# Performance work log

Hardware: AMD Instinct MI355X
Metric: run time of the kernel (lower is better)

Reference implementation:

```python
import jax, jax.numpy as jnp
import numpy as np

VOCAB, HIDDEN, BATCH, SEQ = 32000, 512, 64, 512


def setup_inputs() -> dict:
    key = jax.random.key(0)
    k0, k1, k2, k3, k4, k5 = jax.random.split(key, 6)
    s = 1.0 / np.sqrt(HIDDEN)  # PyTorch LSTMCell init scale
    return {
        "inputs": jax.random.randint(k0, (BATCH, SEQ), 0, VOCAB, dtype=jnp.int64),
        "embedding": jax.random.normal(k1, (VOCAB, HIDDEN), dtype=jnp.float32),
        "W_ih": jax.random.normal(k2, (4 * HIDDEN, HIDDEN), dtype=jnp.float32) * s,
        "W_hh": jax.random.normal(k3, (4 * HIDDEN, HIDDEN), dtype=jnp.float32) * s,
        "b_ih": jax.random.normal(k4, (4 * HIDDEN,), dtype=jnp.float32) * s,
        "b_hh": jax.random.normal(k5, (4 * HIDDEN,), dtype=jnp.float32) * s,
    }


def reference(inputs, embedding, W_ih, W_hh, b_ih, b_hh):
    # Embedding lookup: (B, S, H)
    x = embedding[inputs]
    B, S, H = x.shape
    bias = b_ih + b_hh

    def step(carry, xt):
        h, c = carry
        # gates: (B, 4H); PyTorch LSTMCell gate order i, f, g, o
        gates = xt @ W_ih.T + h @ W_hh.T + bias
        i, f, g, o = jnp.split(gates, 4, axis=-1)
        i = jax.nn.sigmoid(i)
        f = jax.nn.sigmoid(f)
        g = jnp.tanh(g)
        o = jax.nn.sigmoid(o)
        c_new = f * c + i * g
        h_new = o * jnp.tanh(c_new)
        return (h_new, c_new), h_new

    h0 = jnp.zeros((B, H), dtype=x.dtype)
    c0 = jnp.zeros((B, H), dtype=x.dtype)
    (h, c), hs = jax.lax.scan(step, (h0, c0), jnp.swapaxes(x, 0, 1))
    annotations = jnp.swapaxes(hs, 0, 1)  # (B, S, H)
    return annotations, h, c
```

## Files before the change

kernel.cpp:

```cpp
#include <hip/hip_runtime.h>
#include <math.h>

#define B 64
#define S 512
#define H 512
#define G4 2048

typedef __attribute__((ext_vector_type(8))) short bf16x8;
typedef __attribute__((ext_vector_type(4))) float f32x4;

__device__ __forceinline__ float sigmoidf_(float x) {
    return 1.0f / (1.0f + __expf(-x));
}
__device__ __forceinline__ float tanhf_(float x) {
    return 2.0f / (1.0f + __expf(-2.0f * x)) - 1.0f;
}

__device__ __forceinline__ ushort f2bf(float f) {
    union { float f; unsigned int u; } v; v.f = f;
    unsigned int r = v.u + 0x7FFFu + ((v.u >> 16) & 1u);
    return (ushort)(r >> 16);
}
__device__ __forceinline__ float bf2f(ushort s) {
    union { unsigned int u; float f; } v; v.u = ((unsigned int)s) << 16;
    return v.f;
}
__device__ __forceinline__ void split_bf(float x, ushort& hi, ushort& lo) {
    const ushort h = f2bf(x);
    hi = h;
    lo = f2bf(x - bf2f(h));
}

__global__ __launch_bounds__(256)
void w_split(const float* __restrict__ W,
             ushort* __restrict__ Whi,
             ushort* __restrict__ Wlo)
{
    const int i = blockIdx.x * 256 + threadIdx.x;
    const float4 v = reinterpret_cast<const float4*>(W)[i];
    ushort4 hi, lo;
    split_bf(v.x, hi.x, lo.x);
    split_bf(v.y, hi.y, lo.y);
    split_bf(v.z, hi.z, lo.z);
    split_bf(v.w, hi.w, lo.w);
    reinterpret_cast<ushort4*>(Whi)[i] = hi;
    reinterpret_cast<ushort4*>(Wlo)[i] = lo;
}

__global__ __launch_bounds__(256)
void xg_mfma(const int* __restrict__ tokens,
             const float* __restrict__ emb,
             const ushort* __restrict__ Whi,
             const ushort* __restrict__ Wlo,
             const float* __restrict__ b_ih,
             const float* __restrict__ b_hh,
             ushort* __restrict__ xg)
{
    const int mtile = blockIdx.x;
    const int ntile = blockIdx.y;
    const int tid   = threadIdx.x;

    __shared__ ushort Ahi[128][32];
    __shared__ ushort Alo[128][32];
    __shared__ ushort Bhi[128][32];
    __shared__ ushort Blo[128][32];

    const int ar  = tid >> 3;
    const int seg = tid & 7;
    const float* asrc[4];
    #pragma unroll
    for (int i = 0; i < 4; ++i) {
        const int m   = mtile * 128 + ar + i * 32;
        const int tok = tokens[(m & 63) * S + (m >> 6)];
        asrc[i] = emb + (size_t)tok * H + seg * 4;
    }

    const int br = tid >> 2;
    const int bc = (tid & 3) * 8;
    const ushort* bsrc_hi[2];
    const ushort* bsrc_lo[2];
    #pragma unroll
    for (int j = 0; j < 2; ++j) {
        const int n = ntile * 128 + br + j * 64;
        bsrc_hi[j] = Whi + (size_t)n * H + bc;
        bsrc_lo[j] = Wlo + (size_t)n * H + bc;
    }

    const int lane = tid & 63;
    const int wv   = tid >> 6;
    const int wr   = (wv >> 1) * 64;
    const int wc   = (wv & 1) * 64;
    const int fr   = lane & 15;
    const int ks   = lane >> 4;

    f32x4 acc[4][4];
    #pragma unroll
    for (int a = 0; a < 4; ++a)
        #pragma unroll
        for (int c = 0; c < 4; ++c)
            acc[a][c] = (f32x4){0.f, 0.f, 0.f, 0.f};

    for (int kc = 0; kc < 16; ++kc) {
        const int d0 = kc * 32;

        #pragma unroll
        for (int i = 0; i < 4; ++i) {
            const float4 v = *reinterpret_cast<const float4*>(asrc[i] + d0);
            ushort4 hi, lo;
            split_bf(v.x, hi.x, lo.x);
            split_bf(v.y, hi.y, lo.y);
            split_bf(v.z, hi.z, lo.z);
            split_bf(v.w, hi.w, lo.w);
            const int r = ar + i * 32;
            *reinterpret_cast<ushort4*>(&Ahi[r][seg * 4]) = hi;
            *reinterpret_cast<ushort4*>(&Alo[r][seg * 4]) = lo;
        }
        #pragma unroll
        for (int j = 0; j < 2; ++j) {
            const int r = br + j * 64;
            *reinterpret_cast<uint4*>(&Bhi[r][bc]) =
                *reinterpret_cast<const uint4*>(bsrc_hi[j] + d0);
            *reinterpret_cast<uint4*>(&Blo[r][bc]) =
                *reinterpret_cast<const uint4*>(bsrc_lo[j] + d0);
        }
        __syncthreads();

        bf16x8 ah[4], al[4];
        #pragma unroll
        for (int fm = 0; fm < 4; ++fm) {
            ah[fm] = *reinterpret_cast<const bf16x8*>(&Ahi[wr + fm * 16 + fr][ks * 8]);
            al[fm] = *reinterpret_cast<const bf16x8*>(&Alo[wr + fm * 16 + fr][ks * 8]);
        }
        #pragma unroll
        for (int fn = 0; fn < 4; ++fn) {
            const bf16x8 bh = *reinterpret_cast<const bf16x8*>(&Bhi[wc + fn * 16 + fr][ks * 8]);
            const bf16x8 bl = *reinterpret_cast<const bf16x8*>(&Blo[wc + fn * 16 + fr][ks * 8]);
            #pragma unroll
            for (int fm = 0; fm < 4; ++fm) {
                acc[fm][fn] = __builtin_amdgcn_mfma_f32_16x16x32_bf16(ah[fm], bh, acc[fm][fn], 0, 0, 0);
                acc[fm][fn] = __builtin_amdgcn_mfma_f32_16x16x32_bf16(al[fm], bh, acc[fm][fn], 0, 0, 0);
                acc[fm][fn] = __builtin_amdgcn_mfma_f32_16x16x32_bf16(ah[fm], bl, acc[fm][fn], 0, 0, 0);
            }
        }
        __syncthreads();
    }

    #pragma unroll
    for (int fn = 0; fn < 4; ++fn) {
        const int col  = ntile * 128 + wc + fn * 16 + fr;
        const float bias = b_ih[col] + b_hh[col];
        const int gate = col >> 9;
        const int k    = col & 511;
        const int w    = k >> 4;
        const int kl   = k & 15;
        #pragma unroll
        for (int fm = 0; fm < 4; ++fm) {
            const int row = mtile * 128 + wr + fm * 16 + ks * 4;
            const int t   = row >> 6;
            const int b   = row & 63;
            const int g   = b >> 3;
            const int b8  = b & 7;
            ushort4 us;
            us.x = f2bf(acc[fm][fn][0] + bias);
            us.y = f2bf(acc[fm][fn][1] + bias);
            us.z = f2bf(acc[fm][fn][2] + bias);
            us.w = f2bf(acc[fm][fn][3] + bias);
            const size_t idx = ((((size_t)t * 8 + g) * 32 + w) * 512) +
                               gate * 128 + kl * 8 + b8;
            *reinterpret_cast<ushort4*>(&xg[idx]) = us;
        }
    }
}

__global__ __launch_bounds__(256)
void xg_gemm(const int* __restrict__ tokens,
             const float* __restrict__ emb,
             const float* __restrict__ W_ih,
             const float* __restrict__ b_ih,
             const float* __restrict__ b_hh,
             ushort* __restrict__ xg)
{
    const int t      = blockIdx.x;
    const int g_base = blockIdx.y * 128;
    const int tid    = threadIdx.x;

    const int b_ld = tid >> 2;
    const int seg  = tid & 3;
    const int r_w  = tid >> 1;
    const int half = tid & 1;
    const int b0 = (tid & 15) * 4;
    const int g0 = (tid >> 4) * 8;

    const int token = tokens[b_ld * S + t];
    const float4* embrow = reinterpret_cast<const float4*>(emb) + (size_t)token * (H / 4);

    __shared__ float hs[64][64];
    __shared__ float ws[128][68];

    float acc[4][8];
    #pragma unroll
    for (int i = 0; i < 4; ++i)
        #pragma unroll
        for (int j = 0; j < 8; ++j) acc[i][j] = 0.0f;

    for (int kc = 0; kc < 8; ++kc) {
        const int d0 = kc * 64;
        #pragma unroll
        for (int i = 0; i < 4; ++i) {
            const int dl = seg * 16 + i * 4;
            const float4 f = embrow[(d0 >> 2) + seg * 4 + i];
            hs[dl + 0][b_ld] = f.x;
            hs[dl + 1][b_ld] = f.y;
            hs[dl + 2][b_ld] = f.z;
            hs[dl + 3][b_ld] = f.w;
        }
        const float4* wrow = reinterpret_cast<const float4*>(W_ih) +
                             (size_t)(g_base + r_w) * (H / 4) + (d0 >> 2) + half * 8;
        #pragma unroll
        for (int i = 0; i < 8; ++i) {
            *reinterpret_cast<float4*>(&ws[r_w][half * 32 + i * 4]) = wrow[i];
        }
        __syncthreads();

        #pragma unroll
        for (int d4 = 0; d4 < 16; ++d4) {
            const float4 hv0 = *reinterpret_cast<const float4*>(&hs[d4 * 4 + 0][b0]);
            const float4 hv1 = *reinterpret_cast<const float4*>(&hs[d4 * 4 + 1][b0]);
            const float4 hv2 = *reinterpret_cast<const float4*>(&hs[d4 * 4 + 2][b0]);
            const float4 hv3 = *reinterpret_cast<const float4*>(&hs[d4 * 4 + 3][b0]);
            #pragma unroll
            for (int gg = 0; gg < 8; ++gg) {
                const float4 w = *reinterpret_cast<const float4*>(&ws[g0 + gg][d4 * 4]);
                acc[0][gg] += hv0.x * w.x + hv1.x * w.y + hv2.x * w.z + hv3.x * w.w;
                acc[1][gg] += hv0.y * w.x + hv1.y * w.y + hv2.y * w.z + hv3.y * w.w;
                acc[2][gg] += hv0.z * w.x + hv1.z * w.y + hv2.z * w.z + hv3.z * w.w;
                acc[3][gg] += hv0.w * w.x + hv1.w * w.y + hv2.w * w.z + hv3.w * w.w;
            }
        }
        __syncthreads();
    }

    const int grp = b0 >> 3;
    const int b8l = b0 & 7;
    #pragma unroll
    for (int gg = 0; gg < 8; ++gg) {
        const int gcol = g_base + g0 + gg;
        const int gate = gcol >> 9;
        const int k    = gcol & 511;
        const int w    = k >> 4;
        const int kl   = k & 15;
        const float bias = b_ih[gcol] + b_hh[gcol];
        ushort4 us;
        us.x = f2bf(acc[0][gg] + bias);
        us.y = f2bf(acc[1][gg] + bias);
        us.z = f2bf(acc[2][gg] + bias);
        us.w = f2bf(acc[3][gg] + bias);
        const size_t idx = ((((size_t)t * 8 + grp) * 32 + w) * 512) +
                           gate * 128 + kl * 8 + b8l;
        *reinterpret_cast<ushort4*>(&xg[idx]) = us;
    }
}

#define GSTR 4096
#define PSTR 32768

__global__ __launch_bounds__(256)
__attribute__((amdgpu_waves_per_eu(1, 1)))
void lstm_persist_mfma(const ushort* __restrict__ Whh_hi,
                       const ushort* __restrict__ Whh_lo,
                       const ushort* __restrict__ xg,
                       float* __restrict__ hq,
                       unsigned int* __restrict__ bar,
                       float* __restrict__ out)
{
    const int tid  = threadIdx.x;
    const int g    = blockIdx.x & 7;
    const int w    = blockIdx.x >> 3;
    const int k0   = w * 16;
    const int lane = tid & 63;
    const int wv   = tid >> 6;

    unsigned int* bcnt = bar + g * 64;

    const int  bcol   = lane & 15;
    const int  klane  = 4 * wv + (lane >> 4);
    const bool active = bcol < 8;
    const int  b8     = lane & 7;

    const ushort* xg_wg = xg + (((size_t)g * 32 + w) * 512);

    const int ar    = lane & 15;
    const int agate = ar & 3;
    const int ak    = k0 + 4 * wv + (ar >> 2);
    const size_t arow = ((size_t)agate * 512 + ak) * 512 + (size_t)(lane >> 4) * 8;
    bf16x8 afh[16], afl[16];
    #pragma unroll
    for (int ks = 0; ks < 16; ++ks) {
        afh[ks] = *reinterpret_cast<const bf16x8*>(Whh_hi + arow + ks * 32);
        afl[ks] = *reinterpret_cast<const bf16x8*>(Whh_lo + arow + ks * 32);
    }

    __shared__ ushort hs_hi[8 * 512];
    __shared__ ushort hs_lo[8 * 512];

    float c_reg = 0.0f;

    float xv_cur[4] = {0.f, 0.f, 0.f, 0.f};
    if (active) {
        #pragma unroll
        for (int gate = 0; gate < 4; ++gate)
            xv_cur[gate] = bf2f(xg_wg[gate * 128 + klane * 8 + b8]);
    }

    char* hs_hi_c = reinterpret_cast<char*>(hs_hi);
    char* hs_lo_c = reinterpret_cast<char*>(hs_lo);

    for (int t = 0; t < S; ++t) {
        const unsigned long long* hsrc8 = reinterpret_cast<const unsigned long long*>(
            hq + (t & 1) * PSTR + g * GSTR);
        unsigned long long hv[8];
        #pragma unroll
        for (int i = 0; i < 8; ++i)
            hv[i] = __hip_atomic_load(&hsrc8[i * 256 + tid],
                                      __ATOMIC_RELAXED, __HIP_MEMORY_SCOPE_AGENT);
        #pragma unroll
        for (int i = 0; i < 8; ++i) {
            const int e  = 2 * (i * 256 + tid);
            const int bb = e >> 9;
            const int dd = e & 511;
            union { unsigned long long u; float f[2]; } uv; uv.u = hv[i];
            ushort h0, l0, h1, l1;
            split_bf(uv.f[0], h0, l0);
            split_bf(uv.f[1], h1, l1);
            const int byteoff = ((bb << 10) + (dd << 1)) ^ (bb << 4);
            *reinterpret_cast<unsigned int*>(hs_hi_c + byteoff) =
                ((unsigned int)h1 << 16) | (unsigned int)h0;
            *reinterpret_cast<unsigned int*>(hs_lo_c + byteoff) =
                ((unsigned int)l1 << 16) | (unsigned int)l0;
        }
        __syncthreads();

        float xv_nxt[4] = {0.f, 0.f, 0.f, 0.f};
        if (active && t + 1 < S) {
            const ushort* p = xg_wg + (size_t)(t + 1) * (8 * 32 * 512);
            #pragma unroll
            for (int gate = 0; gate < 4; ++gate)
                xv_nxt[gate] = bf2f(p[gate * 128 + klane * 8 + b8]);
        }

        f32x4 a0 = (f32x4){0.f,0.f,0.f,0.f}, a1 = a0, a2 = a0, a3 = a0, a4 = a0, a5 = a0;
        #pragma unroll
        for (int ks = 0; ks < 16; ++ks) {
            const int kbyte = ((b8 << 10) + ((ks * 32 + (lane >> 4) * 8) << 1)) ^ (b8 << 4);
            const bf16x8 bh = *reinterpret_cast<const bf16x8*>(hs_hi_c + kbyte);
            const bf16x8 bl = *reinterpret_cast<const bf16x8*>(hs_lo_c + kbyte);
            if (ks & 1) {
                a1 = __builtin_amdgcn_mfma_f32_16x16x32_bf16(afh[ks], bh, a1, 0, 0, 0);
                a3 = __builtin_amdgcn_mfma_f32_16x16x32_bf16(afl[ks], bh, a3, 0, 0, 0);
                a5 = __builtin_amdgcn_mfma_f32_16x16x32_bf16(afh[ks], bl, a5, 0, 0, 0);
            } else {
                a0 = __builtin_amdgcn_mfma_f32_16x16x32_bf16(afh[ks], bh, a0, 0, 0, 0);
                a2 = __builtin_amdgcn_mfma_f32_16x16x32_bf16(afl[ks], bh, a2, 0, 0, 0);
                a4 = __builtin_amdgcn_mfma_f32_16x16x32_bf16(afh[ks], bl, a4, 0, 0, 0);
            }
        }
        const f32x4 acc = (a0 + a1) + ((a2 + a3) + (a4 + a5));

        float hn = 0.0f, cn = 0.0f;
        if (active) {
            const float ig = sigmoidf_(acc[0] + xv_cur[0]);
            const float fg = sigmoidf_(acc[1] + xv_cur[1]);
            const float gg = tanhf_(acc[2] + xv_cur[2]);
            const float og = sigmoidf_(acc[3] + xv_cur[3]);
            cn = fg * c_reg + ig * gg;
            c_reg = cn;
            hn = og * tanhf_(cn);
            __hip_atomic_store(&hq[((t & 1) ^ 1) * PSTR + g * GSTR + b8 * 512 + k0 + klane],
                               hn, __ATOMIC_RELAXED, __HIP_MEMORY_SCOPE_AGENT);
        }

        __syncthreads();
        if (tid == 0)
            __hip_atomic_fetch_add(bcnt, 1u, __ATOMIC_RELAXED,
                                   __HIP_MEMORY_SCOPE_AGENT);

        if (active) {
            out[((size_t)(g * 8 + b8) * S + t) * H + k0 + klane] = hn;
            if (t == S - 1) {
                const size_t OFF = (size_t)B * S * H;
                out[OFF + (size_t)(g * 8 + b8) * H + k0 + klane] = hn;
                out[OFF + (size_t)B * H + (size_t)(g * 8 + b8) * H + k0 + klane] = cn;
            }
        }

        const unsigned int target = 32u * (unsigned int)(t + 1);
        while (__hip_atomic_load(bcnt, __ATOMIC_RELAXED,
                                 __HIP_MEMORY_SCOPE_AGENT) < target)
            __builtin_amdgcn_s_sleep(2);

        xv_cur[0] = xv_nxt[0]; xv_cur[1] = xv_nxt[1];
        xv_cur[2] = xv_nxt[2]; xv_cur[3] = xv_nxt[3];
    }
}

__global__ __launch_bounds__(256)
__attribute__((amdgpu_waves_per_eu(1, 1)))
void lstm_persist(const float* __restrict__ W_hh,
                  const ushort* __restrict__ xg,
                  float* __restrict__ hq,
                  unsigned int* __restrict__ bar,
                  float* __restrict__ out)
{
    const int tid = threadIdx.x;
    const int g   = blockIdx.x & 7;
    const int w   = blockIdx.x >> 3;
    const int k0  = w * 16;

    const int rp = tid & 31;
    const int d8 = tid >> 5;
    const int d0 = d8 * 64;

    const int b8 = tid >> 4;
    const int kl = tid & 15;

    unsigned int* bcnt = bar + g * 64;

    const ushort* xg_wg = xg + (((size_t)g * 32 + w) * 512);

    float4 wreg[2][16];
    #pragma unroll
    for (int r = 0; r < 2; ++r) {
        const int rl = 2 * rp + r;
        const int grow = (rl >> 4) * H + k0 + (rl & 15);
        const float4* wp = reinterpret_cast<const float4*>(W_hh + (size_t)grow * H + d0);
        #pragma unroll
        for (int i = 0; i < 16; ++i) wreg[r][i] = wp[i];
    }

    __shared__ float hs[8 * 512];
    __shared__ float part[8 * 8 * 64];

    float c_reg = 0.0f;

    float xv_cur[4] = {0.f, 0.f, 0.f, 0.f};
    if (tid < 128) {
        #pragma unroll
        for (int gate = 0; gate < 4; ++gate)
            xv_cur[gate] = bf2f(xg_wg[gate * 128 + kl * 8 + b8]);
    }

    for (int t = 0; t < S; ++t) {
        const unsigned long long* hsrc8 = reinterpret_cast<const unsigned long long*>(
            hq + (t & 1) * PSTR + g * GSTR);
        #pragma unroll
        for (int i = 0; i < 8; ++i) {
            const unsigned long long v = __hip_atomic_load(&hsrc8[i * 256 + tid],
                                                           __ATOMIC_RELAXED,
                                                           __HIP_MEMORY_SCOPE_AGENT);
            reinterpret_cast<unsigned long long*>(hs)[i * 256 + tid] = v;
        }
        __syncthreads();

        float xv_nxt[4] = {0.f, 0.f, 0.f, 0.f};
        if (tid < 128 && t + 1 < S) {
            const ushort* p = xg_wg + (size_t)(t + 1) * (8 * 32 * 512);
            #pragma unroll
            for (int gate = 0; gate < 4; ++gate)
                xv_nxt[gate] = bf2f(p[gate * 128 + kl * 8 + b8]);
        }

        float acc[2][8];
        #pragma unroll
        for (int r = 0; r < 2; ++r)
            #pragma unroll
            for (int b = 0; b < 8; ++b) acc[r][b] = 0.0f;

        #pragma unroll
        for (int b = 0; b < 8; ++b) {
            const float4* h4 = reinterpret_cast<const float4*>(hs + b * 512 + d0);
            #pragma unroll
            for (int i = 0; i < 16; ++i) {
                const float4 hv = h4[i];
                acc[0][b] += wreg[0][i].x * hv.x + wreg[0][i].y * hv.y +
                             wreg[0][i].z * hv.z + wreg[0][i].w * hv.w;
                acc[1][b] += wreg[1][i].x * hv.x + wreg[1][i].y * hv.y +
                             wreg[1][i].z * hv.z + wreg[1][i].w * hv.w;
            }
        }

        #pragma unroll
        for (int r = 0; r < 2; ++r)
            #pragma unroll
            for (int b = 0; b < 8; ++b)
                part[d8 * 512 + b * 64 + 2 * rp + r] = acc[r][b];
        __syncthreads();

        if (tid < 128) {
            float v[4];
            #pragma unroll
            for (int gate = 0; gate < 4; ++gate) {
                const int rl = gate * 16 + kl;
                float s = 0.0f;
                #pragma unroll
                for (int q = 0; q < 8; ++q) s += part[q * 512 + b8 * 64 + rl];
                v[gate] = s + xv_cur[gate];
            }
            const float ig = sigmoidf_(v[0]);
            const float fg = sigmoidf_(v[1]);
            const float gg = tanhf_(v[2]);
            const float og = sigmoidf_(v[3]);

            const float cn = fg * c_reg + ig * gg;
            c_reg = cn;
            const float hn = og * tanhf_(cn);

            __hip_atomic_store(&hq[((t & 1) ^ 1) * PSTR + g * GSTR + b8 * 512 + k0 + kl],
                               hn, __ATOMIC_RELAXED, __HIP_MEMORY_SCOPE_AGENT);
            out[((size_t)(g * 8 + b8) * S + t) * H + k0 + kl] = hn;
            if (t == S - 1) {
                const size_t OFF = (size_t)B * S * H;
                out[OFF + (size_t)(g * 8 + b8) * H + k0 + kl] = hn;
                out[OFF + (size_t)B * H + (size_t)(g * 8 + b8) * H + k0 + kl] = cn;
            }
        }

        __syncthreads();
        if (tid == 0) {
            __hip_atomic_fetch_add(bcnt, 1u, __ATOMIC_RELAXED,
                                   __HIP_MEMORY_SCOPE_AGENT);
            const unsigned int target = 32u * (unsigned int)(t + 1);
            while (__hip_atomic_load(bcnt, __ATOMIC_RELAXED,
                                     __HIP_MEMORY_SCOPE_AGENT) < target)
                __builtin_amdgcn_s_sleep(2);
        }
        __syncthreads();

        xv_cur[0] = xv_nxt[0]; xv_cur[1] = xv_nxt[1];
        xv_cur[2] = xv_nxt[2]; xv_cur[3] = xv_nxt[3];
    }
}

__global__ __launch_bounds__(128)
void lstm_step_fb(const int* __restrict__ tokens,
                  const float* __restrict__ emb,
                  const float* __restrict__ W_ih,
                  const float* __restrict__ W_hh,
                  const float* __restrict__ b_ih,
                  const float* __restrict__ b_hh,
                  const float* __restrict__ h_prev,
                  float* __restrict__ h_next,
                  float* __restrict__ c_st,
                  float* __restrict__ out,
                  int t)
{
    const int tid = threadIdx.x;
    const int b   = tid & 63;
    const int k   = blockIdx.x * 2 + (tid >> 6);
    const int token = tokens[b * S + t];
    const float* xrow = emb + (size_t)token * H;
    const float* hrow = h_prev + b * H;
    float acc[4];
    #pragma unroll
    for (int g = 0; g < 4; ++g) acc[g] = b_ih[g * H + k] + b_hh[g * H + k];
    for (int d = 0; d < H; ++d) {
        const float xv = xrow[d], hv = hrow[d];
        #pragma unroll
        for (int g = 0; g < 4; ++g)
            acc[g] += xv * W_ih[(size_t)(g * H + k) * H + d] + hv * W_hh[(size_t)(g * H + k) * H + d];
    }
    const float ig = sigmoidf_(acc[0]);
    const float fg = sigmoidf_(acc[1]);
    const float gg = tanhf(acc[2]);
    const float og = sigmoidf_(acc[3]);
    const int ck = b * H + k;
    const float cn = fg * c_st[ck] + ig * gg;
    c_st[ck] = cn;
    const float hn = og * tanhf(cn);
    h_next[ck] = hn;
    out[(size_t)b * S * H + (size_t)t * H + k] = hn;
    if (t == S - 1) {
        out[(size_t)B * S * H + ck] = hn;
        out[(size_t)B * S * H + B * H + ck] = cn;
    }
}

extern "C" void kernel_launch(void* const* d_in, const int* in_sizes, int n_in,
                              void* d_out, int out_size, void* d_ws, size_t ws_size,
                              hipStream_t stream)
{
    const int*   tokens = (const int*)d_in[0];
    const float* emb    = (const float*)d_in[1];
    const float* W_ih   = (const float*)d_in[2];
    const float* W_hh   = (const float*)d_in[3];
    const float* b_ih   = (const float*)d_in[4];
    const float* b_hh   = (const float*)d_in[5];
    float* out = (float*)d_out;

    const size_t XG_BYTES  = (size_t)S * G4 * B * 2;
    const size_t HQ_BYTES  = (size_t)2 * PSTR * 4;
    const size_t BAR_BYTES = 8 * 64 * 4;
    const size_t W_BYTES   = (size_t)G4 * H * 2;
    const size_t NEED_OLD  = XG_BYTES + HQ_BYTES + BAR_BYTES;
    const size_t NEED_R1   = NEED_OLD + 2 * W_BYTES;
    const size_t NEED_R2   = NEED_OLD + 4 * W_BYTES;

    if (ws_size >= NEED_R2) {
        ushort* xg = (ushort*)d_ws;
        float*  hq = (float*)((char*)d_ws + XG_BYTES);
        unsigned int* bar = (unsigned int*)((char*)d_ws + XG_BYTES + HQ_BYTES);
        ushort* Wih_hi = (ushort*)((char*)d_ws + NEED_OLD);
        ushort* Wih_lo = Wih_hi + (size_t)G4 * H;
        ushort* Whh_hi = Wih_lo + (size_t)G4 * H;
        ushort* Whh_lo = Whh_hi + (size_t)G4 * H;

        (void)hipMemsetAsync(hq, 0, HQ_BYTES + BAR_BYTES, stream);

        w_split<<<dim3((G4 * H / 4) / 256), dim3(256), 0, stream>>>(W_ih, Wih_hi, Wih_lo);
        w_split<<<dim3((G4 * H / 4) / 256), dim3(256), 0, stream>>>(W_hh, Whh_hi, Whh_lo);

        xg_mfma<<<dim3(256, 16), dim3(256), 0, stream>>>(
            tokens, emb, Wih_hi, Wih_lo, b_ih, b_hh, xg);

        lstm_persist_mfma<<<dim3(256), dim3(256), 0, stream>>>(
            Whh_hi, Whh_lo, xg, hq, bar, out);
    } else if (ws_size >= NEED_R1) {
        ushort* xg = (ushort*)d_ws;
        float*  hq = (float*)((char*)d_ws + XG_BYTES);
        unsigned int* bar = (unsigned int*)((char*)d_ws + XG_BYTES + HQ_BYTES);
        ushort* Wih_hi = (ushort*)((char*)d_ws + NEED_OLD);
        ushort* Wih_lo = Wih_hi + (size_t)G4 * H;

        (void)hipMemsetAsync(hq, 0, HQ_BYTES + BAR_BYTES, stream);

        w_split<<<dim3((G4 * H / 4) / 256), dim3(256), 0, stream>>>(W_ih, Wih_hi, Wih_lo);

        xg_mfma<<<dim3(256, 16), dim3(256), 0, stream>>>(
            tokens, emb, Wih_hi, Wih_lo, b_ih, b_hh, xg);

        lstm_persist<<<dim3(256), dim3(256), 0, stream>>>(W_hh, xg, hq, bar, out);
    } else if (ws_size >= NEED_OLD) {
        ushort* xg = (ushort*)d_ws;
        float*  hq = (float*)((char*)d_ws + XG_BYTES);
        unsigned int* bar = (unsigned int*)((char*)d_ws + XG_BYTES + HQ_BYTES);

        (void)hipMemsetAsync(hq, 0, HQ_BYTES + BAR_BYTES, stream);

        xg_gemm<<<dim3(S, 16), dim3(256), 0, stream>>>(tokens, emb, W_ih, b_ih, b_hh, xg);

        lstm_persist<<<dim3(256), dim3(256), 0, stream>>>(W_hh, xg, hq, bar, out);
    } else {
        float* c_st = (float*)d_ws;
        float* h0   = c_st + B * H;
        float* h1   = h0 + B * H;
        (void)hipMemsetAsync(d_ws, 0, (size_t)3 * B * H * sizeof(float), stream);
        for (int t = 0; t < S; ++t) {
            const float* hp = (t & 1) ? h1 : h0;
            float*       hn = (t & 1) ? h0 : h1;
            lstm_step_fb<<<dim3(256), dim3(128), 0, stream>>>(
                tokens, emb, W_ih, W_hh, b_ih, b_hh, hp, hn, c_st, out, t);
        }
    }
}
```

Measured before the change: 1.972 ms.

## Fuse input projection into persistent LSTM kernel, dropping the precomputed xg buffer

Removes the separate xg_mfma pre-GEMM and its large bf16 gate buffer. Each persistent block now keeps W_ih hi/lo fragments in registers, gathers the next token's embedding rows into double-buffered LDS, and computes x·W_ih with split-bf16 MFMAs inside every timestep. The two weight-split launches are merged into one 2D launch. The barrier spin moves after the output stores. This trades a bulk parallel GEMM and global round trip for extra MFMA work, register pressure and embedding gather latency on the sequential critical path.

```diff
diff --git a/kernel.cpp b/kernel.cpp
--- a/kernel.cpp
+++ b/kernel.cpp
@@ -32,10 +32,12 @@
 }
 
 __global__ __launch_bounds__(256)
-void w_split(const float* __restrict__ W,
-             ushort* __restrict__ Whi,
-             ushort* __restrict__ Wlo)
+void w_split2(const float* __restrict__ W0, ushort* __restrict__ W0hi, ushort* __restrict__ W0lo,
+              const float* __restrict__ W1, ushort* __restrict__ W1hi, ushort* __restrict__ W1lo)
 {
+    const float* W = blockIdx.y ? W1 : W0;
+    ushort* Whi = blockIdx.y ? W1hi : W0hi;
+    ushort* Wlo = blockIdx.y ? W1lo : W0lo;
     const int i = blockIdx.x * 256 + threadIdx.x;
     const float4 v = reinterpret_cast<const float4*>(W)[i];
     ushort4 hi, lo;
@@ -172,97 +174,211 @@
     }
 }
 
-__global__ __launch_bounds__(256)
-void xg_gemm(const int* __restrict__ tokens,
-             const float* __restrict__ emb,
-             const float* __restrict__ W_ih,
-             const float* __restrict__ b_ih,
-             const float* __restrict__ b_hh,
-             ushort* __restrict__ xg)
-{
-    const int t      = blockIdx.x;
-    const int g_base = blockIdx.y * 128;
-    const int tid    = threadIdx.x;
-
-    const int b_ld = tid >> 2;
-    const int seg  = tid & 3;
-    const int r_w  = tid >> 1;
-    const int half = tid & 1;
-    const int b0 = (tid & 15) * 4;
-    const int g0 = (tid >> 4) * 8;
-
-    const int token = tokens[b_ld * S + t];
-    const float4* embrow = reinterpret_cast<const float4*>(emb) + (size_t)token * (H / 4);
-
-    __shared__ float hs[64][64];
-    __shared__ float ws[128][68];
-
-    float acc[4][8];
-    #pragma unroll
-    for (int i = 0; i < 4; ++i)
-        #pragma unroll
-        for (int j = 0; j < 8; ++j) acc[i][j] = 0.0f;
-
-    for (int kc = 0; kc < 8; ++kc) {
-        const int d0 = kc * 64;
-        #pragma unroll
-        for (int i = 0; i < 4; ++i) {
-            const int dl = seg * 16 + i * 4;
-            const float4 f = embrow[(d0 >> 2) + seg * 4 + i];
-            hs[dl + 0][b_ld] = f.x;
-            hs[dl + 1][b_ld] = f.y;
-            hs[dl + 2][b_ld] = f.z;
-            hs[dl + 3][b_ld] = f.w;
-        }
-        const float4* wrow = reinterpret_cast<const float4*>(W_ih) +
-                             (size_t)(g_base + r_w) * (H / 4) + (d0 >> 2) + half * 8;
-        #pragma unroll
-        for (int i = 0; i < 8; ++i) {
-            *reinterpret_cast<float4*>(&ws[r_w][half * 32 + i * 4]) = wrow[i];
-        }
-        __syncthreads();
-
-        #pragma unroll
-        for (int d4 = 0; d4 < 16; ++d4) {
-            const float4 hv0 = *reinterpret_cast<const float4*>(&hs[d4 * 4 + 0][b0]);
-            const float4 hv1 = *reinterpret_cast<const float4*>(&hs[d4 * 4 + 1][b0]);
-            const float4 hv2 = *reinterpret_cast<const float4*>(&hs[d4 * 4 + 2][b0]);
-            const float4 hv3 = *reinterpret_cast<const float4*>(&hs[d4 * 4 + 3][b0]);
-            #pragma unroll
-            for (int gg = 0; gg < 8; ++gg) {
-                const float4 w = *reinterpret_cast<const float4*>(&ws[g0 + gg][d4 * 4]);
-                acc[0][gg] += hv0.x * w.x + hv1.x * w.y + hv2.x * w.z + hv3.x * w.w;
-                acc[1][gg] += hv0.y * w.x + hv1.y * w.y + hv2.y * w.z + hv3.y * w.w;
-                acc[2][gg] += hv0.z * w.x + hv1.z * w.y + hv2.z * w.z + hv3.z * w.w;
-                acc[3][gg] += hv0.w * w.x + hv1.w * w.y + hv2.w * w.z + hv3.w * w.w;
-            }
-        }
-        __syncthreads();
-    }
-
-    const int grp = b0 >> 3;
-    const int b8l = b0 & 7;
-    #pragma unroll
-    for (int gg = 0; gg < 8; ++gg) {
-        const int gcol = g_base + g0 + gg;
-        const int gate = gcol >> 9;
-        const int k    = gcol & 511;
-        const int w    = k >> 4;
-        const int kl   = k & 15;
-        const float bias = b_ih[gcol] + b_hh[gcol];
-        ushort4 us;
-        us.x = f2bf(acc[0][gg] + bias);
-        us.y = f2bf(acc[1][gg] + bias);
-        us.z = f2bf(acc[2][gg] + bias);
-        us.w = f2bf(acc[3][gg] + bias);
-        const size_t idx = ((((size_t)t * 8 + grp) * 32 + w) * 512) +
-                           gate * 128 + kl * 8 + b8l;
-        *reinterpret_cast<ushort4*>(&xg[idx]) = us;
-    }
-}
-
 #define GSTR 4096
 #define PSTR 32768
+
+__global__ __launch_bounds__(256)
+__attribute__((amdgpu_waves_per_eu(1, 1)))
+void lstm_persist_fused(const ushort* __restrict__ Whh_hi,
+                        const ushort* __restrict__ Whh_lo,
+                        const ushort* __restrict__ Wih_hi,
+                        const ushort* __restrict__ Wih_lo,
+                        const int*    __restrict__ tokens,
+                        const float*  __restrict__ emb,
+                        const float*  __restrict__ b_ih,
+                        const float*  __restrict__ b_hh,
+                        float* __restrict__ hq,
+                        unsigned int* __restrict__ bar,
+                        float* __restrict__ out)
+{
+    const int tid  = threadIdx.x;
+    const int g    = blockIdx.x & 7;
+    const int w    = blockIdx.x >> 3;
+    const int k0   = w * 16;
+    const int lane = tid & 63;
+    const int wv   = tid >> 6;
+
+    const int  bcol   = lane & 15;
+    const int  klane  = 4 * wv + (lane >> 4);
+    const bool active = bcol < 8;
+    const int  b8     = lane & 7;
+
+    unsigned int* bcnt = bar + g * 64;
+
+    const int ar    = lane & 15;
+    const int agate = ar & 3;
+    const int ak    = k0 + 4 * wv + (ar >> 2);
+    const size_t arow = ((size_t)agate * 512 + ak) * 512 + (size_t)(lane >> 4) * 8;
+    bf16x8 afh[16], afl[16], wfh[16], wfl[16];
+    #pragma unroll
+    for (int ks = 0; ks < 16; ++ks) {
+        afh[ks] = *reinterpret_cast<const bf16x8*>(Whh_hi + arow + ks * 32);
+        afl[ks] = *reinterpret_cast<const bf16x8*>(Whh_lo + arow + ks * 32);
+        wfh[ks] = *reinterpret_cast<const bf16x8*>(Wih_hi + arow + ks * 32);
+        wfl[ks] = *reinterpret_cast<const bf16x8*>(Wih_lo + arow + ks * 32);
+    }
+
+    float bias[4] = {0.f, 0.f, 0.f, 0.f};
+    if (active) {
+        #pragma unroll
+        for (int j = 0; j < 4; ++j) {
+            const int col = j * 512 + k0 + klane;
+            bias[j] = b_ih[col] + b_hh[col];
+        }
+    }
+
+    __shared__ ushort hs_hi[8 * 512];
+    __shared__ ushort hs_lo[8 * 512];
+    __shared__ ushort em_hi[2][8 * 512];
+    __shared__ ushort em_lo[2][8 * 512];
+
+    char* hs_hi_c = reinterpret_cast<char*>(hs_hi);
+    char* hs_lo_c = reinterpret_cast<char*>(hs_lo);
+    char* em_hi_c = reinterpret_cast<char*>(em_hi);
+    char* em_lo_c = reinterpret_cast<char*>(em_lo);
+
+    float c_reg = 0.0f;
+
+    {
+        #pragma unroll
+        for (int i = 0; i < 8; ++i) {
+            const int tok = tokens[(g * 8 + i) * S + 0];
+            const float2 v = *reinterpret_cast<const float2*>(
+                emb + (size_t)tok * H + 2 * tid);
+            ushort h0, l0, h1, l1;
+            split_bf(v.x, h0, l0);
+            split_bf(v.y, h1, l1);
+            const int byteoff = ((i << 10) + (tid << 2)) ^ (i << 4);
+            *reinterpret_cast<unsigned int*>(em_hi_c + byteoff) =
+                ((unsigned int)h1 << 16) | (unsigned int)h0;
+            *reinterpret_cast<unsigned int*>(em_lo_c + byteoff) =
+                ((unsigned int)l1 << 16) | (unsigned int)l0;
+        }
+    }
+    __syncthreads();
+
+    for (int t = 0; t < S; ++t) {
+        const int ep = (t & 1) * 8192;
+
+        f32x4 x0 = (f32x4){0.f,0.f,0.f,0.f}, x1 = x0, x2 = x0, x3 = x0, x4 = x0, x5 = x0;
+        #pragma unroll
+        for (int ks = 0; ks < 16; ++ks) {
+            const int kbyte = (((b8 << 10) + ((ks * 32 + (lane >> 4) * 8) << 1)) ^ (b8 << 4)) + ep;
+            const bf16x8 bh = *reinterpret_cast<const bf16x8*>(em_hi_c + kbyte);
+            const bf16x8 bl = *reinterpret_cast<const bf16x8*>(em_lo_c + kbyte);
+            if (ks & 1) {
+                x1 = __builtin_amdgcn_mfma_f32_16x16x32_bf16(wfh[ks], bh, x1, 0, 0, 0);
+                x3 = __builtin_amdgcn_mfma_f32_16x16x32_bf16(wfl[ks], bh, x3, 0, 0, 0);
+                x5 = __builtin_amdgcn_mfma_f32_16x16x32_bf16(wfh[ks], bl, x5, 0, 0, 0);
+            } else {
+                x0 = __builtin_amdgcn_mfma_f32_16x16x32_bf16(wfh[ks], bh, x0, 0, 0, 0);
+                x2 = __builtin_amdgcn_mfma_f32_16x16x32_bf16(wfl[ks], bh, x2, 0, 0, 0);
+                x4 = __builtin_amdgcn_mfma_f32_16x16x32_bf16(wfh[ks], bl, x4, 0, 0, 0);
+            }
+        }
+        const f32x4 xga = (x0 + x1) + ((x2 + x3) + (x4 + x5));
+        float xv[4];
+        #pragma unroll
+        for (int j = 0; j < 4; ++j) xv[j] = xga[j] + bias[j];
+
+        const unsigned long long* hsrc8 = reinterpret_cast<const unsigned long long*>(
+            hq + (t & 1) * PSTR + g * GSTR);
+        unsigned long long hv[8];
+        #pragma unroll
+        for (int i = 0; i < 8; ++i)
+            hv[i] = __hip_atomic_load(&hsrc8[i * 256 + tid],
+                                      __ATOMIC_RELAXED, __HIP_MEMORY_SCOPE_AGENT);
+        #pragma unroll
+        for (int i = 0; i < 8; ++i) {
+            const int e  = 2 * (i * 256 + tid);
+            const int bb = e >> 9;
+            const int dd = e & 511;
+            union { unsigned long long u; float f[2]; } uv; uv.u = hv[i];
+            ushort h0, l0, h1, l1;
+            split_bf(uv.f[0], h0, l0);
+            split_bf(uv.f[1], h1, l1);
+            const int byteoff = ((bb << 10) + (dd << 1)) ^ (bb << 4);
+            *reinterpret_cast<unsigned int*>(hs_hi_c + byteoff) =
+                ((unsigned int)h1 << 16) | (unsigned int)h0;
+            *reinterpret_cast<unsigned int*>(hs_lo_c + byteoff) =
+                ((unsigned int)l1 << 16) | (unsigned int)l0;
+        }
+
+        float2 ev[8];
+        if (t + 1 < S) {
+            #pragma unroll
+            for (int i = 0; i < 8; ++i) {
+                const int tok = tokens[(g * 8 + i) * S + (t + 1)];
+                ev[i] = *reinterpret_cast<const float2*>(
+                    emb + (size_t)tok * H + 2 * tid);
+            }
+        }
+        __syncthreads();
+
+        f32x4 a0 = (f32x4){0.f,0.f,0.f,0.f}, a1 = a0, a2 = a0, a3 = a0, a4 = a0, a5 = a0;
+        #pragma unroll
+        for (int ks = 0; ks < 16; ++ks) {
+            const int kbyte = ((b8 << 10) + ((ks * 32 + (lane >> 4) * 8) << 1)) ^ (b8 << 4);
+            const bf16x8 bh = *reinterpret_cast<const bf16x8*>(hs_hi_c + kbyte);
+            const bf16x8 bl = *reinterpret_cast<const bf16x8*>(hs_lo_c + kbyte);
+            if (ks & 1) {
+                a1 = __builtin_amdgcn_mfma_f32_16x16x32_bf16(afh[ks], bh, a1, 0, 0, 0);
+                a3 = __builtin_amdgcn_mfma_f32_16x16x32_bf16(afl[ks], bh, a3, 0, 0, 0);
+                a5 = __builtin_amdgcn_mfma_f32_16x16x32_bf16(afh[ks], bl, a5, 0, 0, 0);
+            } else {
+                a0 = __builtin_amdgcn_mfma_f32_16x16x32_bf16(afh[ks], bh, a0, 0, 0, 0);
+                a2 = __builtin_amdgcn_mfma_f32_16x16x32_bf16(afl[ks], bh, a2, 0, 0, 0);
+                a4 = __builtin_amdgcn_mfma_f32_16x16x32_bf16(afh[ks], bl, a4, 0, 0, 0);
+            }
+        }
+        const f32x4 acc = (a0 + a1) + ((a2 + a3) + (a4 + a5));
+
+        float hn = 0.0f, cn = 0.0f;
+        if (active) {
+            const float ig = sigmoidf_(acc[0] + xv[0]);
+            const float fg = sigmoidf_(acc[1] + xv[1]);
+            const float gg = tanhf_(acc[2] + xv[2]);
+            const float og = sigmoidf_(acc[3] + xv[3]);
+            cn = fg * c_reg + ig * gg;
+            c_reg = cn;
+            hn = og * tanhf_(cn);
+            __hip_atomic_store(&hq[((t & 1) ^ 1) * PSTR + g * GSTR + b8 * 512 + k0 + klane],
+                               hn, __ATOMIC_RELAXED, __HIP_MEMORY_SCOPE_AGENT);
+            out[((size_t)(g * 8 + b8) * S + t) * H + k0 + klane] = hn;
+            if (t == S - 1) {
+                const size_t OFF = (size_t)B * S * H;
+                out[OFF + (size_t)(g * 8 + b8) * H + k0 + klane] = hn;
+                out[OFF + (size_t)B * H + (size_t)(g * 8 + b8) * H + k0 + klane] = cn;
+            }
+        }
+
+        if (t + 1 < S) {
+            const int epn = ((t + 1) & 1) * 8192;
+            #pragma unroll
+            for (int i = 0; i < 8; ++i) {
+                ushort h0, l0, h1, l1;
+                split_bf(ev[i].x, h0, l0);
+                split_bf(ev[i].y, h1, l1);
+                const int byteoff = (((i << 10) + (tid << 2)) ^ (i << 4)) + epn;
+                *reinterpret_cast<unsigned int*>(em_hi_c + byteoff) =
+                    ((unsigned int)h1 << 16) | (unsigned int)h0;
+                *reinterpret_cast<unsigned int*>(em_lo_c + byteoff) =
+                    ((unsigned int)l1 << 16) | (unsigned int)l0;
+            }
+        }
+
+        __syncthreads();
+        if (tid == 0) {
+            __hip_atomic_fetch_add(bcnt, 1u, __ATOMIC_RELAXED,
+                                   __HIP_MEMORY_SCOPE_AGENT);
+            const unsigned int target = 32u * (unsigned int)(t + 1);
+            while (__hip_atomic_load(bcnt, __ATOMIC_RELAXED,
+                                     __HIP_MEMORY_SCOPE_AGENT) < target)
+                __builtin_amdgcn_s_sleep(2);
+        }
+        __syncthreads();
+    }
+}
 
 __global__ __launch_bounds__(256)
 __attribute__((amdgpu_waves_per_eu(1, 1)))
@@ -280,13 +396,12 @@
     const int lane = tid & 63;
     const int wv   = tid >> 6;
 
-    unsigned int* bcnt = bar + g * 64;
-
     const int  bcol   = lane & 15;
     const int  klane  = 4 * wv + (lane >> 4);
     const bool active = bcol < 8;
     const int  b8     = lane & 7;
 
+    unsigned int* bcnt = bar + g * 64;
     const ushort* xg_wg = xg + (((size_t)g * 32 + w) * 512);
 
     const int ar    = lane & 15;
@@ -377,150 +492,11 @@
             hn = og * tanhf_(cn);
             __hip_atomic_store(&hq[((t & 1) ^ 1) * PSTR + g * GSTR + b8 * 512 + k0 + klane],
                                hn, __ATOMIC_RELAXED, __HIP_MEMORY_SCOPE_AGENT);
-        }
-
-        __syncthreads();
-        if (tid == 0)
-            __hip_atomic_fetch_add(bcnt, 1u, __ATOMIC_RELAXED,
-                                   __HIP_MEMORY_SCOPE_AGENT);
-
-        if (active) {
             out[((size_t)(g * 8 + b8) * S + t) * H + k0 + klane] = hn;
             if (t == S - 1) {
                 const size_t OFF = (size_t)B * S * H;
                 out[OFF + (size_t)(g * 8 + b8) * H + k0 + klane] = hn;
                 out[OFF + (size_t)B * H + (size_t)(g * 8 + b8) * H + k0 + klane] = cn;
-            }
-        }
-
-        const unsigned int target = 32u * (unsigned int)(t + 1);
-        while (__hip_atomic_load(bcnt, __ATOMIC_RELAXED,
-                                 __HIP_MEMORY_SCOPE_AGENT) < target)
-            __builtin_amdgcn_s_sleep(2);
-
-        xv_cur[0] = xv_nxt[0]; xv_cur[1] = xv_nxt[1];
-        xv_cur[2] = xv_nxt[2]; xv_cur[3] = xv_nxt[3];
-    }
-}
-
-__global__ __launch_bounds__(256)
-__attribute__((amdgpu_waves_per_eu(1, 1)))
-void lstm_persist(const float* __restrict__ W_hh,
-                  const ushort* __restrict__ xg,
-                  float* __restrict__ hq,
-                  unsigned int* __restrict__ bar,
-                  float* __restrict__ out)
-{
-    const int tid = threadIdx.x;
-    const int g   = blockIdx.x & 7;
-    const int w   = blockIdx.x >> 3;
-    const int k0  = w * 16;
-
-    const int rp = tid & 31;
-    const int d8 = tid >> 5;
-    const int d0 = d8 * 64;
-
-    const int b8 = tid >> 4;
-    const int kl = tid & 15;
-
-    unsigned int* bcnt = bar + g * 64;
-
-    const ushort* xg_wg = xg + (((size_t)g * 32 + w) * 512);
-
-    float4 wreg[2][16];
-    #pragma unroll
-    for (int r = 0; r < 2; ++r) {
-        const int rl = 2 * rp + r;
-        const int grow = (rl >> 4) * H + k0 + (rl & 15);
-        const float4* wp = reinterpret_cast<const float4*>(W_hh + (size_t)grow * H + d0);
-        #pragma unroll
-        for (int i = 0; i < 16; ++i) wreg[r][i] = wp[i];
-    }
-
-    __shared__ float hs[8 * 512];
-    __shared__ float part[8 * 8 * 64];
-
-    float c_reg = 0.0f;
-
-    float xv_cur[4] = {0.f, 0.f, 0.f, 0.f};
-    if (tid < 128) {
-        #pragma unroll
-        for (int gate = 0; gate < 4; ++gate)
-            xv_cur[gate] = bf2f(xg_wg[gate * 128 + kl * 8 + b8]);
-    }
-
-    for (int t = 0; t < S; ++t) {
-        const unsigned long long* hsrc8 = reinterpret_cast<const unsigned long long*>(
-            hq + (t & 1) * PSTR + g * GSTR);
-        #pragma unroll
-        for (int i = 0; i < 8; ++i) {
-            const unsigned long long v = __hip_atomic_load(&hsrc8[i * 256 + tid],
-                                                           __ATOMIC_RELAXED,
-                                                           __HIP_MEMORY_SCOPE_AGENT);
-            reinterpret_cast<unsigned long long*>(hs)[i * 256 + tid] = v;
-        }
-        __syncthreads();
-
-        float xv_nxt[4] = {0.f, 0.f, 0.f, 0.f};
-        if (tid < 128 && t + 1 < S) {
-            const ushort* p = xg_wg + (size_t)(t + 1) * (8 * 32 * 512);
-            #pragma unroll
-            for (int gate = 0; gate < 4; ++gate)
-                xv_nxt[gate] = bf2f(p[gate * 128 + kl * 8 + b8]);
-        }
-
-        float acc[2][8];
-        #pragma unroll
-        for (int r = 0; r < 2; ++r)
-            #pragma unroll
-            for (int b = 0; b < 8; ++b) acc[r][b] = 0.0f;
-
-        #pragma unroll
-        for (int b = 0; b < 8; ++b) {
-            const float4* h4 = reinterpret_cast<const float4*>(hs + b * 512 + d0);
-            #pragma unroll
-            for (int i = 0; i < 16; ++i) {
-                const float4 hv = h4[i];
-                acc[0][b] += wreg[0][i].x * hv.x + wreg[0][i].y * hv.y +
-                             wreg[0][i].z * hv.z + wreg[0][i].w * hv.w;
-                acc[1][b] += wreg[1][i].x * hv.x + wreg[1][i].y * hv.y +
-                             wreg[1][i].z * hv.z + wreg[1][i].w * hv.w;
-            }
-        }
-
-        #pragma unroll
-        for (int r = 0; r < 2; ++r)
-            #pragma unroll
-            for (int b = 0; b < 8; ++b)
-                part[d8 * 512 + b * 64 + 2 * rp + r] = acc[r][b];
-        __syncthreads();
-
-        if (tid < 128) {
-            float v[4];
-            #pragma unroll
-            for (int gate = 0; gate < 4; ++gate) {
-                const int rl = gate * 16 + kl;
-                float s = 0.0f;
-                #pragma unroll
-                for (int q = 0; q < 8; ++q) s += part[q * 512 + b8 * 64 + rl];
-                v[gate] = s + xv_cur[gate];
-            }
-            const float ig = sigmoidf_(v[0]);
-            const float fg = sigmoidf_(v[1]);
-            const float gg = tanhf_(v[2]);
-            const float og = sigmoidf_(v[3]);
-
-            const float cn = fg * c_reg + ig * gg;
-            c_reg = cn;
-            const float hn = og * tanhf_(cn);
-
-            __hip_atomic_store(&hq[((t & 1) ^ 1) * PSTR + g * GSTR + b8 * 512 + k0 + kl],
-                               hn, __ATOMIC_RELAXED, __HIP_MEMORY_SCOPE_AGENT);
-            out[((size_t)(g * 8 + b8) * S + t) * H + k0 + kl] = hn;
-            if (t == S - 1) {
-                const size_t OFF = (size_t)B * S * H;
-                out[OFF + (size_t)(g * 8 + b8) * H + k0 + kl] = hn;
-                out[OFF + (size_t)B * H + (size_t)(g * 8 + b8) * H + k0 + kl] = cn;
             }
         }
 
@@ -596,58 +572,32 @@
     const float* b_hh   = (const float*)d_in[5];
     float* out = (float*)d_out;
 
-    const size_t XG_BYTES  = (size_t)S * G4 * B * 2;
-    const size_t HQ_BYTES  = (size_t)2 * PSTR * 4;
-    const size_t BAR_BYTES = 8 * 64 * 4;
-    const size_t W_BYTES   = (size_t)G4 * H * 2;
-    const size_t NEED_OLD  = XG_BYTES + HQ_BYTES + BAR_BYTES;
-    const size_t NEED_R1   = NEED_OLD + 2 * W_BYTES;
-    const size_t NEED_R2   = NEED_OLD + 4 * W_BYTES;
-
-    if (ws_size >= NEED_R2) {
-        ushort* xg = (ushort*)d_ws;
-        float*  hq = (float*)((char*)d_ws + XG_BYTES);
-        unsigned int* bar = (unsigned int*)((char*)d_ws + XG_BYTES + HQ_BYTES);
-        ushort* Wih_hi = (ushort*)((char*)d_ws + NEED_OLD);
+    const size_t HQ_BYTES   = (size_t)2 * PSTR * 4;
+    const size_t BAR_BYTES  = 8 * 64 * 4;
+    const size_t W_BYTES    = (size_t)G4 * H * 2;
+    const size_t XG_BYTES   = (size_t)S * G4 * B * 2;
+    const size_t NEED_FUSED = HQ_BYTES + BAR_BYTES + 4 * W_BYTES;
+    const size_t NEED_R2    = XG_BYTES + HQ_BYTES + BAR_BYTES + 4 * W_BYTES;
+
+    if (ws_size >= NEED_FUSED && ws_size < NEED_R2) {
+    }
+
+    if (ws_size >= NEED_FUSED) {
+        float* hq = (float*)d_ws;
+        unsigned int* bar = (unsigned int*)((char*)d_ws + HQ_BYTES);
+        ushort* Wih_hi = (ushort*)((char*)d_ws + HQ_BYTES + BAR_BYTES);
         ushort* Wih_lo = Wih_hi + (size_t)G4 * H;
         ushort* Whh_hi = Wih_lo + (size_t)G4 * H;
         ushort* Whh_lo = Whh_hi + (size_t)G4 * H;
 
         (void)hipMemsetAsync(hq, 0, HQ_BYTES + BAR_BYTES, stream);
 
-        w_split<<<dim3((G4 * H / 4) / 256), dim3(256), 0, stream>>>(W_ih, Wih_hi, Wih_lo);
-        w_split<<<dim3((G4 * H / 4) / 256), dim3(256), 0, stream>>>(W_hh, Whh_hi, Whh_lo);
-
-        xg_mfma<<<dim3(256, 16), dim3(256), 0, stream>>>(
-            tokens, emb, Wih_hi, Wih_lo, b_ih, b_hh, xg);
-
-        lstm_persist_mfma<<<dim3(256), dim3(256), 0, stream>>>(
-            Whh_hi, Whh_lo, xg, hq, bar, out);
-    } else if (ws_size >= NEED_R1) {
-        ushort* xg = (ushort*)d_ws;
-        float*  hq = (float*)((char*)d_ws + XG_BYTES);
-        unsigned int* bar = (unsigned int*)((char*)d_ws + XG_BYTES + HQ_BYTES);
-        ushort* Wih_hi = (ushort*)((char*)d_ws + NEED_OLD);
-        ushort* Wih_lo = Wih_hi + (size_t)G4 * H;
-
-        (void)hipMemsetAsync(hq, 0, HQ_BYTES + BAR_BYTES, stream);
-
-        w_split<<<dim3((G4 * H / 4) / 256), dim3(256), 0, stream>>>(W_ih, Wih_hi, Wih_lo);
-
-        xg_mfma<<<dim3(256, 16), dim3(256), 0, stream>>>(
-            tokens, emb, Wih_hi, Wih_lo, b_ih, b_hh, xg);
-
-        lstm_persist<<<dim3(256), dim3(256), 0, stream>>>(W_hh, xg, hq, bar, out);
-    } else if (ws_size >= NEED_OLD) {
-        ushort* xg = (ushort*)d_ws;
-        float*  hq = (float*)((char*)d_ws + XG_BYTES);
-        unsigned int* bar = (unsigned int*)((char*)d_ws + XG_BYTES + HQ_BYTES);
-
-        (void)hipMemsetAsync(hq, 0, HQ_BYTES + BAR_BYTES, stream);
-
-        xg_gemm<<<dim3(S, 16), dim3(256), 0, stream>>>(tokens, emb, W_ih, b_ih, b_hh, xg);
-
-        lstm_persist<<<dim3(256), dim3(256), 0, stream>>>(W_hh, xg, hq, bar, out);
+        w_split2<<<dim3((G4 * H / 4) / 256, 2), dim3(256), 0, stream>>>(
+            W_ih, Wih_hi, Wih_lo, W_hh, Whh_hi, Whh_lo);
+
+        lstm_persist_fused<<<dim3(256), dim3(256), 0, stream>>>(
+            Whh_hi, Whh_lo, Wih_hi, Wih_lo, tokens, emb, b_ih, b_hh,
+            hq, bar, out);
     } else {
         float* c_st = (float*)d_ws;
         float* h0   = c_st + B * H;
```

Result: slower. 2.454 ms (+24.4%).
